# Kernel tuning notes

Hardware: AMD Instinct MI355X
Metric: run time of the kernel (lower is better)

## Reference

```python
import jax, jax.numpy as jnp
import numpy as np

B, S, T1, V = 32, 60, 60, 50000   # batch, post len, response len (decoder runs T1-1 steps), vocab
E, A, H, ATT, DI = 300, 300, 512, 512, 512  # word emb, affect emb, rnn hidden, attention size, decoder input


def setup_inputs() -> dict:
    key = jax.random.key(0)
    ks = jax.random.split(key, 20)
    p = lambda i, shape: jax.random.normal(ks[i], shape, jnp.float32) * 0.02
    z = lambda n: jnp.zeros((n,), jnp.float32)
    return {
        'posts': jax.random.randint(ks[0], (B, S), 0, V),
        'responses': jax.random.randint(ks[1], (B, T1), 0, V),
        'len_posts': jnp.full((B,), S, jnp.int32),
        'emb': p(2, (V, E)), 'affect_emb': p(3, (V, A)),
        'enc_Wi': p(4, (3 * H, E)), 'enc_Wh': p(5, (3 * H, H)), 'enc_bi': z(3 * H), 'enc_bh': z(3 * H),
        'aff_Wi': p(6, (3 * H, A)), 'aff_Wh': p(7, (3 * H, H)), 'aff_bi': z(3 * H), 'aff_bh': z(3 * H),
        'Wp': p(8, (H, 2 * H)), 'bp': z(H),
        'Wl': p(9, (DI, E + H + ATT)), 'bl': z(DI),
        'dec_Wi': p(10, (3 * H, DI)), 'dec_Wh': p(11, (3 * H, H)), 'dec_bi': z(3 * H), 'dec_bh': z(3 * H),
        'Wa': p(12, (H, H)), 'Wc': p(13, (ATT, H)), 'bc': z(ATT),
        'Wv': p(14, (V, H + ATT)), 'bv': z(V),
    }


def _gru_cell(x, h, Wi, Wh, bi, bh):
    gi = x @ Wi.T + bi
    gh = h @ Wh.T + bh
    ir, iz, inn = jnp.split(gi, 3, -1)
    hr, hz, hn = jnp.split(gh, 3, -1)
    r = jax.nn.sigmoid(ir + hr)
    zg = jax.nn.sigmoid(iz + hz)
    n = jnp.tanh(inn + r * hn)
    return (1.0 - zg) * n + zg * h


def _gru_seq(xs, h0, Wi, Wh, bi, bh):
    # xs: [S, B, in] -> (outputs [S,B,H], h_last [B,H])
    def step(h, x):
        h2 = _gru_cell(x, h, Wi, Wh, bi, bh)
        return h2, h2
    hT, ys = jax.lax.scan(step, h0, xs)
    return ys, hT


def reference(posts, responses, len_posts, emb, affect_emb,
              enc_Wi, enc_Wh, enc_bi, enc_bh,
              aff_Wi, aff_Wh, aff_bi, aff_bh,
              Wp, bp, Wl, bl,
              dec_Wi, dec_Wh, dec_bi, dec_bh,
              Wa, Wc, bc, Wv, bv):
    embed_posts = emb[posts]            # [B,S,E]
    affect_posts = affect_emb[posts]    # [B,S,A]
    h0 = jnp.zeros((posts.shape[0], H), embed_posts.dtype)

    _, state_encoder = _gru_seq(embed_posts.transpose(1, 0, 2), h0, enc_Wi, enc_Wh, enc_bi, enc_bh)
    out_affect, state_affect = _gru_seq(affect_posts.transpose(1, 0, 2), h0, aff_Wi, aff_Wh, aff_bi, aff_bh)
    context_affect = out_affect[-1]     # [B,H] (all lengths == S)
    K = out_affect.transpose(1, 0, 2)   # [B,S,H] attention keys/values

    # PrepareState: Linear + tanh on concat of both encoder final states
    state0 = jnp.tanh(jnp.concatenate([state_encoder, state_affect], -1) @ Wp.T + bp)

    dec_in = emb[responses[:, :-1]].transpose(1, 0, 2)  # [T,B,E]
    init_attn = jnp.zeros((posts.shape[0], ATT), embed_posts.dtype)

    def dec_step(carry, x_emb):
        h, attn = carry
        x = jnp.concatenate([x_emb, context_affect, attn], -1) @ Wl.T + bl
        h = _gru_cell(x, h, dec_Wi, dec_Wh, dec_bi, dec_bh)
        scores = jnp.einsum('bd,bsd->bs', h @ Wa, K)        # Luong 'general'
        w = jax.nn.softmax(scores, -1)
        ctx = jnp.einsum('bs,bsd->bd', w, K)
        attn = jnp.tanh(ctx @ Wc.T + bc)
        return (h, attn), (jnp.concatenate([h, attn], -1), w)

    _, (outs, weights) = jax.lax.scan(dec_step, (state0, init_attn), dec_in)
    outs = outs.transpose(1, 0, 2)          # [B,T,H+ATT]
    weights = weights.transpose(1, 0, 2)    # [B,T,S]
    output_vocab = jax.nn.softmax(outs @ Wv.T + bv, -1)  # [B,T,V]
    return output_vocab, weights
```

## Files before the change

### kernel.cpp

```cpp
#include <hip/hip_runtime.h>

typedef unsigned int uint32;
typedef unsigned short u16;
typedef unsigned long long u64;
typedef __attribute__((ext_vector_type(8))) short bf8;
typedef __attribute__((ext_vector_type(4))) float f4;
typedef __attribute__((ext_vector_type(4))) uint32 u32x4;

#define DEV static __device__ __forceinline__

DEV f4 MFMA(bf8 a, bf8 b, f4 c) {
  return __builtin_amdgcn_mfma_f32_16x16x32_bf16(a, b, c, 0, 0, 0);
}
DEV u16 f2bf(float f) {
  uint32 u = __float_as_uint(f);
  return (u16)((u + 0x7FFFu + ((u >> 16) & 1u)) >> 16);
}
DEV float bf2f(u16 h) { return __uint_as_float(((uint32)h) << 16); }
DEV float bfLO(uint32 u) { return __uint_as_float(u << 16); }
DEV float bfHI(uint32 u) { return __uint_as_float(u & 0xFFFF0000u); }
DEV float sigmoid_(float x) { return 1.f / (1.f + __expf(-x)); }
DEV float tanh_(float x) {
  float cx = fminf(fmaxf(x, -15.f), 15.f);
  float e = __expf(2.f * cx);
  return (e - 1.f) / (e + 1.f);
}

DEV u64 ldA64(const void* p) {
  return __hip_atomic_load((u64*)p, __ATOMIC_RELAXED, __HIP_MEMORY_SCOPE_AGENT);
}
DEV void stA64(void* p, u64 v) {
  __hip_atomic_store((u64*)p, v, __ATOMIC_RELAXED, __HIP_MEMORY_SCOPE_AGENT);
}
DEV void stA32(int* p, int v) {
  __hip_atomic_store(p, v, __ATOMIC_RELAXED, __HIP_MEMORY_SCOPE_AGENT);
}
DEV bf8 pk_frag(u64 lo, u64 hi) {
  u32x4 v = {(uint32)lo, (uint32)(lo >> 32), (uint32)hi, (uint32)(hi >> 32)};
  return __builtin_bit_cast(bf8, v);
}

DEV void wait_vm0() { asm volatile("s_waitcnt vmcnt(0)" ::: "memory"); }
DEV void wait_slots(const int* slots, int n, int tgt) {
  const int lane = threadIdx.x & 63;
  for (int i = 0; i < (1 << 20); ++i) {
    int v = 0x7fffffff;
    if (lane < n)
      v = __hip_atomic_load((int*)(slots + lane), __ATOMIC_RELAXED,
                            __HIP_MEMORY_SCOPE_AGENT);
    if (__all(v >= tgt)) return;
    __builtin_amdgcn_s_sleep(1);
  }
}

namespace L {
constexpr size_t o_flags  = 0;
constexpr size_t o_rowsum = 4096;
constexpr size_t o_bcomb  = 11776;
constexpr size_t o_gistat = 17920;
constexpr size_t o_xbuf   = 214528;
constexpr size_t o_henc   = 345600;
constexpr size_t o_haff   = 411136;
constexpr size_t o_cat    = 476672;
constexpr size_t o_Kbuf   = 542208;
constexpr size_t o_KA     = 2508288;
constexpr size_t o_embP   = 4474368;
constexpr size_t o_embA   = 5703168;
constexpr size_t o_embD   = 6931968;
constexpr size_t o_encWi  = 8140288;
constexpr size_t o_affWi  = 9123328;
constexpr size_t o_Whe    = 10106368;
constexpr size_t o_Wha    = 11679232;
constexpr size_t o_decWi  = 13252096;
constexpr size_t o_WlT    = 14824960;
constexpr size_t o_Wa     = 16184832;
constexpr size_t o_Wp     = 16709120;
constexpr size_t o_wq     = 17757696;
constexpr size_t o_Wcomb  = 18281984;
constexpr size_t o_WdE    = 26441216;
constexpr size_t o_WdA    = 27424256;
constexpr size_t o_Wd2    = 28997120;
constexpr size_t o_giE    = 32142848;
constexpr size_t o_giA    = 43939328;
constexpr size_t o_giD    = 55735808;
constexpr size_t o_outsB  = 67335680;
constexpr size_t o_WvB    = 71267840;
constexpr size_t WS_FULL  = 174028288;
constexpr size_t WOFF = 94400000;
}

__global__ __launch_bounds__(256) void kp_gather(
    const int* __restrict__ posts, const int* __restrict__ resp,
    const float* __restrict__ emb, const float* __restrict__ aemb, char* ws)
{
  using namespace L;
  const int gid = blockIdx.x * 256 + threadIdx.x;
  const int r = gid / 320, e = gid - r * 320;
  u16* embP = (u16*)(ws + o_embP);
  u16* embA = (u16*)(ws + o_embA);
  u16* embD = (u16*)(ws + o_embD);
  if (r < 1920) {
    const int b = r & 31, s = r >> 5;
    const int tok = posts[b * 60 + s];
    embP[r * 320 + e] = f2bf(e < 300 ? emb[(size_t)tok * 300 + e] : 0.f);
    embA[r * 320 + e] = f2bf(e < 300 ? aemb[(size_t)tok * 300 + e] : 0.f);
  } else if (r < 3808) {
    const int r2 = r - 1920;
    const int b = r2 & 31, t = r2 >> 5;
    const int tok = resp[b * 60 + t];
    embD[r2 * 320 + e] = f2bf(e < 300 ? emb[(size_t)tok * 300 + e] : 0.f);
  }
}

__global__ __launch_bounds__(256) void kp_wconv(
    const float* __restrict__ encWi, const float* __restrict__ affWi,
    const float* __restrict__ encWh, const float* __restrict__ affWh,
    const float* __restrict__ dWi, const float* __restrict__ Wl,
    const float* __restrict__ Wa, const float* __restrict__ Wp,
    const float* __restrict__ Wc, char* ws)
{
  using namespace L;
  long gid = (long)blockIdx.x * 256 + threadIdx.x;
  if (gid < 983040) {
    const int g = gid >= 491520;
    const long u = gid - (g ? 491520 : 0);
    const int n = (int)(u / 320), e = (int)(u - (long)n * 320);
    const float* src = g ? affWi : encWi;
    u16* dst = (u16*)(ws + (g ? o_affWi : o_encWi));
    dst[u] = f2bf(e < 300 ? src[(size_t)n * 300 + e] : 0.f);
    return;
  }
  gid -= 983040;
  if (gid < 2359296) {
    const int g = (int)(gid / 786432);
    const long u = gid - (long)g * 786432;
    const float* src = g == 0 ? encWh : (g == 1 ? affWh : dWi);
    u16* dst = (u16*)(ws + (g == 0 ? o_Whe : (g == 1 ? o_Wha : o_decWi)));
    dst[u] = f2bf(src[u]);
    return;
  }
  gid -= 2359296;
  if (gid < 679936) {
    const int j = (int)(gid >> 9), k = (int)(gid & 511);
    ((u16*)(ws + o_WlT))[gid] = f2bf(j < 1324 ? Wl[(size_t)k * 1324 + j] : 0.f);
    return;
  }
  gid -= 679936;
  if (gid < 262144) { ((u16*)(ws + o_Wa))[gid] = f2bf(Wa[gid]); return; }
  gid -= 262144;
  if (gid < 524288) { ((u16*)(ws + o_Wp))[gid] = f2bf(Wp[gid]); return; }
  gid -= 524288;
  if (gid < 131072) {
    const int q = (int)(gid & 3), j = (int)((gid >> 2) & 511), g4 = (int)(gid >> 11);
    const int d0 = g4 * 8 + q * 2;
    const uint32 lo = f2bf(Wc[(size_t)j * 512 + d0]);
    const uint32 hi = f2bf(Wc[(size_t)j * 512 + d0 + 1]);
    ((uint32*)(ws + o_wq))[gid] = lo | (hi << 16);
    return;
  }
  gid -= 131072;
  if (gid < 2944) {
    if (gid < 1024) ((uint32*)(ws + o_flags))[gid] = 0;
    else ((uint32*)(ws + o_rowsum))[gid - 1024] = 0;
    return;
  }
  gid -= 2944;
  if (gid < 49152) {
    if (gid < 16384) ((uint32*)(ws + o_outsB + (size_t)1888 * 1024 * 2))[gid] = 0;
    else if (gid < 32768) ((uint32*)(ws + o_henc))[gid - 16384] = 0;
    else ((uint32*)(ws + o_haff))[gid - 32768] = 0;
  }
}

__global__ __launch_bounds__(256) void kp_bcomb(
    const float* __restrict__ dWi, const float* __restrict__ bl,
    const float* __restrict__ dbi, char* ws)
{
  const int i = blockIdx.x * 256 + threadIdx.x;
  if (i >= 1536) return;
  float a = dbi[i];
  for (int k = 0; k < 512; ++k) a += dWi[(size_t)i * 512 + k] * bl[k];
  ((float*)(ws + L::o_bcomb))[i] = a;
}

__global__ __launch_bounds__(256) void kp_wv(const float* __restrict__ Wv, char* ws)
{
  const long gid = (long)blockIdx.x * 256 + threadIdx.x;
  const int r = (int)(gid >> 8), q = (int)(gid & 255);
  u16* WvB = (u16*)(ws + L::o_WvB);
  uint2 o;
  if (r < 50000) {
    const float4 f = *(const float4*)(Wv + (size_t)r * 1024 + q * 4);
    o.x = (uint32)f2bf(f.x) | ((uint32)f2bf(f.y) << 16);
    o.y = (uint32)f2bf(f.z) | ((uint32)f2bf(f.w) << 16);
  } else { o.x = 0u; o.y = 0u; }
  *(uint2*)(WvB + (size_t)r * 1024 + q * 4) = o;
}

__global__ __launch_bounds__(256) void kp_pack2(
    const float* __restrict__ Wcomb, const float* __restrict__ dWh, char* ws)
{
  using namespace L;
  long gid = (long)blockIdx.x * 256 + threadIdx.x;
  if (gid < 491520) {
    const int n = (int)(gid / 320), e = (int)(gid - (long)n * 320);
    ((u16*)(ws + o_WdE))[gid] = f2bf(e < 300 ? Wcomb[(size_t)n * 1328 + e] : 0.f);
    return;
  }
  gid -= 491520;
  if (gid < 786432) {
    const int n = (int)(gid >> 9), k = (int)(gid & 511);
    ((u16*)(ws + o_WdA))[gid] = f2bf(Wcomb[(size_t)n * 1328 + 300 + k]);
    return;
  }
  gid -= 786432;
  if (gid < 1572864) {
    const int n = (int)(gid >> 10), k = (int)(gid & 1023);
    const float v = (k < 512) ? Wcomb[(size_t)n * 1328 + 812 + k]
                              : dWh[(size_t)n * 512 + (k - 512)];
    ((u16*)(ws + o_Wd2))[gid] = f2bf(v);
  }
}

__global__ __launch_bounds__(256) void k_gemm_nt(
    const u16* __restrict__ A, const u16* __restrict__ Bm,
    float* __restrict__ C, const float* __restrict__ bias,
    const int M, const int N, const int Kp)
{
  const int mt = blockIdx.x, cb = blockIdx.y;
  const int w = threadIdx.x >> 6, lane = threadIdx.x & 63;
  const int l15 = lane & 15, lhi = lane >> 4;
  const u16* arow = A + (size_t)(mt * 16 + l15) * Kp + lhi * 8;
  const int c0 = cb * 256 + w * 64;
  f4 acc[4];
#pragma unroll
  for (int nn = 0; nn < 4; ++nn) acc[nn] = (f4){0.f, 0.f, 0.f, 0.f};
  for (int k = 0; k < Kp; k += 32) {
    const bf8 a = *(const bf8*)(arow + k);
#pragma unroll
    for (int nn = 0; nn < 4; ++nn) {
      const int cs = c0 + nn * 16;
      if (cs < N) {
        const bf8 b = *(const bf8*)(Bm + (size_t)(cs + l15) * Kp + k + lhi * 8);
        acc[nn] = MFMA(a, b, acc[nn]);
      }
    }
  }
#pragma unroll
  for (int nn = 0; nn < 4; ++nn) {
    const int cs = c0 + nn * 16;
    if (cs >= N) continue;
    const int c = cs + l15;
    const float bb = bias ? bias[c] : 0.f;
#pragma unroll
    for (int j = 0; j < 4; ++j) {
      const int r = mt * 16 + lhi * 4 + j;
      C[(size_t)r * N + c] = acc[nn][j] + bb;
    }
  }
}

__global__ __launch_bounds__(256, 1) void k_enc(
    char* __restrict__ ws, const float* __restrict__ enc_bh,
    const float* __restrict__ aff_bh)
{
  using namespace L;
  const int tid = threadIdx.x, blk = blockIdx.x;
  const int wave = tid >> 6, lane = tid & 63;
  const int l15 = lane & 15, lhi = lane >> 4;
  const int g = blk >> 5;
  const bool act = wave < 2;
  int* flags = (int*)(ws + o_flags);
  int* slotE = flags + 128 + g * 64;
  const u16* Wh = (const u16*)(ws + (g ? o_Wha : o_Whe));
  const float* gi = (const float*)(ws + (g ? o_giA : o_giE));
  const float* bh = g ? aff_bh : enc_bh;
  u16* hbuf = (u16*)(ws + (g ? o_haff : o_henc));
  u16* cat = (u16*)(ws + o_cat);
  u16* Kb = (u16*)(ws + o_Kbuf);

  const int wid = (blk & 31) * 2 + (wave & 1);
  const int btile = wid >> 5, ctile = wid & 31;
  const int bl = btile * 16 + l15;
  const int c0 = ctile * 16 + lhi * 4;
  const u16* wr0 = Wh + (size_t)(ctile * 16 + l15) * 512 + lhi * 8;
  const u16* wr1 = wr0 + (size_t)512 * 512;
  const u16* wr2 = wr1 + (size_t)512 * 512;
  f4 bhr4 = {0.f, 0.f, 0.f, 0.f}, bhz4 = bhr4, bhn4 = bhr4;
  if (act) {
    bhr4 = *(const f4*)(bh + c0);
    bhz4 = *(const f4*)(bh + 512 + c0);
    bhn4 = *(const f4*)(bh + 1024 + c0);
  }
  for (int s = 0; s < 60; ++s) {
    const u16* hin = hbuf + (s & 1) * (32 * 512);
    u16* hout = hbuf + ((s & 1) ^ 1) * (32 * 512);
    if (act) {
      const u16* brow = hin + bl * 512 + lhi * 8;
      u64 flo[16], fhi[16];
#pragma unroll
      for (int kk = 0; kk < 16; ++kk) {
        flo[kk] = ldA64(brow + kk * 32);
        fhi[kk] = ldA64(brow + kk * 32 + 4);
      }
      const u64 hq = ldA64(hin + bl * 512 + c0);
      f4 ar = {0.f, 0.f, 0.f, 0.f}, az = ar, an = ar;
#pragma unroll
      for (int kk = 0; kk < 16; ++kk) {
        const bf8 hf = pk_frag(flo[kk], fhi[kk]);
        ar = MFMA(*(const bf8*)(wr0 + kk * 32), hf, ar);
        az = MFMA(*(const bf8*)(wr1 + kk * 32), hf, az);
        an = MFMA(*(const bf8*)(wr2 + kk * 32), hf, an);
      }
      const float* gr = gi + (size_t)(s * 32 + bl) * 1536;
      const f4 g0 = *(const f4*)(gr + c0);
      const f4 g1 = *(const f4*)(gr + 512 + c0);
      const f4 g2 = *(const f4*)(gr + 1024 + c0);
      u64 pk = 0;
#pragma unroll
      for (int j = 0; j < 4; ++j) {
        const float r = sigmoid_(g0[j] + ar[j] + bhr4[j]);
        const float z = sigmoid_(g1[j] + az[j] + bhz4[j]);
        const float n = tanh_(g2[j] + r * (an[j] + bhn4[j]));
        const float hold = bf2f((u16)(hq >> (16 * j)));
        pk |= (u64)f2bf((1.f - z) * n + z * hold) << (16 * j);
      }
      stA64(hout + bl * 512 + c0, pk);
      if (g) *(u64*)(Kb + (size_t)(s * 32 + bl) * 512 + c0) = pk;
      if (s == 59) *(u64*)(cat + bl * 1024 + g * 512 + c0) = pk;
    }
    wait_vm0();
    __syncthreads();
    if (tid == 0) stA32(&slotE[blk & 31], s + 1);
    if (wave == 2) wait_slots(slotE, 32, s + 1);
    __syncthreads();
  }
}

__global__ __launch_bounds__(256) void k_mid(char* __restrict__ ws,
                                             const float* __restrict__ bp)
{
  using namespace L;
  const int tid = threadIdx.x, blk = blockIdx.x;
  const int wave = tid >> 6, lane = tid & 63;
  const int l15 = lane & 15, lhi = lane >> 4;
  u16* xb = (u16*)(ws + o_xbuf);
  u16* cat = (u16*)(ws + o_cat);
  u16* Kb = (u16*)(ws + o_Kbuf);

  if (blk < 16) {
    const u16* Wp_ = (const u16*)(ws + o_Wp);
    const int wid = blk * 4 + wave;
    const int btile = wid >> 5, ctile = wid & 31;
    const int bl = btile * 16 + l15;
    const int c0 = ctile * 16 + lhi * 4;
    const u16* arow = Wp_ + (size_t)(ctile * 16 + l15) * 1024 + lhi * 8;
    const u16* brow = cat + bl * 1024 + lhi * 8;
    f4 acc = {0.f, 0.f, 0.f, 0.f};
    for (int k = 0; k < 1024; k += 32)
      acc = MFMA(*(const bf8*)(arow + k), *(const bf8*)(brow + k), acc);
    const f4 bp4 = *(const f4*)(bp + c0);
    u64 pk = 0;
#pragma unroll
    for (int j = 0; j < 4; ++j)
      pk |= (u64)f2bf(tanh_(acc[j] + bp4[j])) << (16 * j);
    *(u64*)(xb + bl * 1024 + 512 + c0) = pk;
    *(u64*)(xb + bl * 1024 + c0) = 0;
  } else if (blk < 32) {
    const u16* WdA = (const u16*)(ws + o_WdA);
    const float* bco = (const float*)(ws + o_bcomb);
    float* gst = (float*)(ws + o_gistat);
    const int wid = (blk - 16) * 4 + wave;
    const int btile = wid >> 5, ctb = wid & 31;
    const int bl = btile * 16 + l15;
    const int c0 = ctb * 16 + lhi * 4;
    const u16* brow = cat + bl * 1024 + 512 + lhi * 8;
    const u16* a0p = WdA + (size_t)(ctb * 16 + l15) * 512 + lhi * 8;
    const u16* a1p = a0p + (size_t)512 * 512;
    const u16* a2p = a1p + (size_t)512 * 512;
    f4 a0 = {0.f, 0.f, 0.f, 0.f}, a1 = a0, a2 = a0;
    for (int k = 0; k < 512; k += 32) {
      const bf8 bfr = *(const bf8*)(brow + k);
      a0 = MFMA(*(const bf8*)(a0p + k), bfr, a0);
      a1 = MFMA(*(const bf8*)(a1p + k), bfr, a1);
      a2 = MFMA(*(const bf8*)(a2p + k), bfr, a2);
    }
    const f4 v0 = *(const f4*)(bco + c0);
    const f4 v1 = *(const f4*)(bco + 512 + c0);
    const f4 v2 = *(const f4*)(bco + 1024 + c0);
    *(f4*)(gst + bl * 1536 + c0) = a0 + v0;
    *(f4*)(gst + bl * 1536 + 512 + c0) = a1 + v1;
    *(f4*)(gst + bl * 1536 + 1024 + c0) = a2 + v2;
  } else {
    const u16* Wa_ = (const u16*)(ws + o_Wa);
    u16* KAp = (u16*)(ws + o_KA);
    const int widK = (blk - 32) * 4 + wave;
    for (int task = widK; task < 3840; task += 192) {
      const int mt = task >> 5, ct = task & 31;
      const int m = mt * 16 + l15;
      const int c0 = ct * 16 + lhi * 4;
      const u16* arow = Wa_ + (size_t)(ct * 16 + l15) * 512 + lhi * 8;
      const u16* brow = Kb + (size_t)m * 512 + lhi * 8;
      f4 acc = {0.f, 0.f, 0.f, 0.f};
      for (int k = 0; k < 512; k += 32)
        acc = MFMA(*(const bf8*)(arow + k), *(const bf8*)(brow + k), acc);
      u64 pk = 0;
#pragma unroll
      for (int j = 0; j < 4; ++j) pk |= (u64)f2bf(acc[j]) << (16 * j);
      *(u64*)(KAp + (size_t)m * 512 + c0) = pk;
    }
  }
}

__global__ __launch_bounds__(256, 1) void k_dec(
    char* __restrict__ ws, float* __restrict__ out,
    const float* __restrict__ dec_bh, const float* __restrict__ bc)
{
  using namespace L;
  const int tid = threadIdx.x, blk = blockIdx.x;
  const int wave = tid >> 6, lane = tid & 63;
  const int l15 = lane & 15, lhi = lane >> 4;
  int* flags = (int*)(ws + o_flags);
  int* slotA = flags;
  int* slotB = flags + 64;

  __shared__ float hsm[512];
  __shared__ float ctxs[512];
  __shared__ float scb[64];
  __shared__ float wsb[64];
  __shared__ u16 attn_sm[256];

  u16* xb = (u16*)(ws + o_xbuf);
  u16* outs = (u16*)(ws + o_outsB);

  if (blk < 32) {
    const bool act = wave < 2;
    const u16* Wd2 = (const u16*)(ws + o_Wd2);
    const float* gst = (const float*)(ws + o_gistat);
    const float* gD = (const float*)(ws + o_giD);
    const int wid = (blk & 31) * 2 + (wave & 1);
    const int btile = wid >> 5, ctile = wid & 31;
    const int bl = btile * 16 + l15;
    const int c0 = ctile * 16 + lhi * 4;
    const u16* wr = Wd2 + (size_t)(ctile * 16 + l15) * 1024 + lhi * 8;
    const u16* wz = wr + (size_t)512 * 1024;
    const u16* wn = wz + (size_t)512 * 1024;
    f4 bhr4 = {0.f, 0.f, 0.f, 0.f}, bhz4 = bhr4, bhn4 = bhr4;
    f4 s0 = bhr4, s1 = bhr4, s2 = bhr4;
    if (act) {
      bhr4 = *(const f4*)(dec_bh + c0);
      bhz4 = *(const f4*)(dec_bh + 512 + c0);
      bhn4 = *(const f4*)(dec_bh + 1024 + c0);
      s0 = *(const f4*)(gst + bl * 1536 + c0);
      s1 = *(const f4*)(gst + bl * 1536 + 512 + c0);
      s2 = *(const f4*)(gst + bl * 1536 + 1024 + c0);
    }
    for (int t = 0; t < 59; ++t) {
      const u16* xin = xb + (t & 1) * (32 * 1024);
      u16* xout = xb + ((t & 1) ^ 1) * (32 * 1024);
      const u16* brow = xin + bl * 1024 + lhi * 8;
      f4 ar = {0.f, 0.f, 0.f, 0.f}, az = ar, anx = ar, anh = ar;
      u64 hq = 0;
      f4 d0 = ar, d1 = ar, d2 = ar;
      if (t) {
        if (wave == 2) wait_slots(slotA, 32, t);
        __syncthreads();
      }
      if (act) {
        u64 flo[16], fhi[16];
#pragma unroll
        for (int kk = 0; kk < 16; ++kk) {
          flo[kk] = ldA64(brow + (16 + kk) * 32);
          fhi[kk] = ldA64(brow + (16 + kk) * 32 + 4);
        }
        hq = ldA64(xin + bl * 1024 + 512 + c0);
        const float* g2p = gD + (size_t)(t * 32 + bl) * 1536;
        d0 = *(const f4*)(g2p + c0);
        d1 = *(const f4*)(g2p + 512 + c0);
        d2 = *(const f4*)(g2p + 1024 + c0);
#pragma unroll
        for (int kk = 0; kk < 16; ++kk) {
          const bf8 xf = pk_frag(flo[kk], fhi[kk]);
          ar = MFMA(*(const bf8*)(wr + (16 + kk) * 32), xf, ar);
          az = MFMA(*(const bf8*)(wz + (16 + kk) * 32), xf, az);
          anh = MFMA(*(const bf8*)(wn + (16 + kk) * 32), xf, anh);
        }
      }
      if (t) {
        if (wave == 2) wait_slots(slotB, 64, t);
        __syncthreads();
      }
      if (act) {
        u64 glo[16], ghi[16];
#pragma unroll
        for (int kk = 0; kk < 16; ++kk) {
          glo[kk] = ldA64(brow + kk * 32);
          ghi[kk] = ldA64(brow + kk * 32 + 4);
        }
#pragma unroll
        for (int kk = 0; kk < 16; ++kk) {
          const bf8 xf = pk_frag(glo[kk], ghi[kk]);
          ar = MFMA(*(const bf8*)(wr + kk * 32), xf, ar);
          az = MFMA(*(const bf8*)(wz + kk * 32), xf, az);
          anx = MFMA(*(const bf8*)(wn + kk * 32), xf, anx);
        }
        u64 pk = 0;
#pragma unroll
        for (int j = 0; j < 4; ++j) {
          const float r = sigmoid_(s0[j] + d0[j] + ar[j] + bhr4[j]);
          const float z = sigmoid_(s1[j] + d1[j] + az[j] + bhz4[j]);
          const float n = tanh_(s2[j] + d2[j] + anx[j] + r * (anh[j] + bhn4[j]));
          const float hold = bf2f((u16)(hq >> (16 * j)));
          pk |= (u64)f2bf((1.f - z) * n + z * hold) << (16 * j);
        }
        stA64(xout + bl * 1024 + 512 + c0, pk);
        *(u64*)(outs + (size_t)(bl * 59 + t) * 1024 + c0) = pk;
      }
      wait_vm0();
      __syncthreads();
      if (tid == 0) stA32(&slotA[blk], t + 1);
    }
  } else {
    const int idx = blk - 32;
    const int b = idx >> 1, half = idx & 1;
    const u16* KAp = (const u16*)(ws + o_KA);
    const u16* Kb = (const u16*)(ws + o_Kbuf);
    const uint4* wq = (const uint4*)(ws + o_wq);
    for (int t = 0; t < 59; ++t) {
      if (wave == 0) wait_slots(slotA, 32, t + 1);
      __syncthreads();
      const u16* xcur = xb + ((t & 1) ^ 1) * (32 * 1024);
      if (tid < 128) {
        const u64 hv = ldA64(xcur + b * 1024 + 512 + tid * 4);
        const uint32 w0 = (uint32)hv, w1 = (uint32)(hv >> 32);
        hsm[tid * 4 + 0] = bfLO(w0);
        hsm[tid * 4 + 1] = bfHI(w0);
        hsm[tid * 4 + 2] = bfLO(w1);
        hsm[tid * 4 + 3] = bfHI(w1);
      }
      __syncthreads();
      if (tid < 240) {
        const int s = tid >> 2, q = tid & 3;
        const u16* kr = KAp + (size_t)(s * 32 + b) * 512 + q * 128;
        const float* hq = &hsm[q * 128];
        float acc0 = 0.f, acc1 = 0.f;
#pragma unroll 4
        for (int i = 0; i < 128; i += 8) {
          const uint2 k4 = *(const uint2*)(kr + i);
          const uint2 k5 = *(const uint2*)(kr + i + 4);
          const float4 h4 = *(const float4*)(hq + i);
          const float4 h5 = *(const float4*)(hq + i + 4);
          acc0 += h4.x * bfLO(k4.x) + h4.y * bfHI(k4.x)
                + h4.z * bfLO(k4.y) + h4.w * bfHI(k4.y);
          acc1 += h5.x * bfLO(k5.x) + h5.y * bfHI(k5.x)
                + h5.z * bfLO(k5.y) + h5.w * bfHI(k5.y);
        }
        float acc = acc0 + acc1;
        acc += __shfl_xor(acc, 1);
        acc += __shfl_xor(acc, 2);
        if ((tid & 3) == 0) scb[s] = acc;
      }
      __syncthreads();
      if (tid < 64) {
        const float v = (tid < 60) ? scb[tid] : -1e30f;
        float m = v;
#pragma unroll
        for (int d = 1; d < 64; d <<= 1) m = fmaxf(m, __shfl_xor(m, d));
        const float e = (tid < 60) ? __expf(v - m) : 0.f;
        float sm = e;
#pragma unroll
        for (int d = 1; d < 64; d <<= 1) sm += __shfl_xor(sm, d);
        const float w = e / sm;
        if (tid < 60) {
          wsb[tid] = w;
          if (half == 0) out[WOFF + (size_t)(b * 59 + t) * 60 + tid] = w;
        }
      }
      __syncthreads();
      {
        float c0a = 0.f, c0b = 0.f, c1a = 0.f, c1b = 0.f;
#pragma unroll 2
        for (int s = 0; s < 60; s += 2) {
          const float w0 = wsb[s], w1 = wsb[s + 1];
          const u16* kr0 = Kb + (size_t)(s * 32 + b) * 512;
          const u16* kr1 = Kb + (size_t)((s + 1) * 32 + b) * 512;
          c0a += w0 * bf2f(kr0[tid]);
          c1a += w0 * bf2f(kr0[tid + 256]);
          c0b += w1 * bf2f(kr1[tid]);
          c1b += w1 * bf2f(kr1[tid + 256]);
        }
        ctxs[tid] = c0a + c0b;
        ctxs[tid + 256] = c1a + c1b;
      }
      __syncthreads();
      const int jj = half * 256 + tid;
      float faa[4] = {0.f, 0.f, 0.f, 0.f};
      float fbb[4] = {0.f, 0.f, 0.f, 0.f};
#pragma unroll 4
      for (int g4 = 0; g4 < 64; ++g4) {
        const uint4 wv4 = wq[g4 * 512 + jj];
        const float4 ca = *(const float4*)&ctxs[g4 * 8];
        const float4 cb2 = *(const float4*)&ctxs[g4 * 8 + 4];
        faa[g4 & 3] += ca.x * bfLO(wv4.x) + ca.y * bfHI(wv4.x)
                     + ca.z * bfLO(wv4.y) + ca.w * bfHI(wv4.y);
        fbb[g4 & 3] += cb2.x * bfLO(wv4.z) + cb2.y * bfHI(wv4.z)
                     + cb2.z * bfLO(wv4.w) + cb2.w * bfHI(wv4.w);
      }
      const float fa = bc[jj] + faa[0] + faa[1] + faa[2] + faa[3]
                     + fbb[0] + fbb[1] + fbb[2] + fbb[3];
      attn_sm[tid] = f2bf(tanh_(fa));
      __syncthreads();
      if (tid < 64) {
        u16* xout = xb + ((t & 1) ^ 1) * (32 * 1024);
        const u64 pk = (u64)attn_sm[tid * 4] | ((u64)attn_sm[tid * 4 + 1] << 16)
                     | ((u64)attn_sm[tid * 4 + 2] << 32) | ((u64)attn_sm[tid * 4 + 3] << 48);
        const int cc = half * 256 + tid * 4;
        stA64(xout + b * 1024 + cc, pk);
        *(u64*)(outs + (size_t)(b * 59 + t) * 1024 + 512 + cc) = pk;
      }
      wait_vm0();
      __syncthreads();
      if (tid == 0) stA32(&slotB[idx], t + 1);
    }
  }
}

__global__ __launch_bounds__(512, 2) void k_vocab2(
    const u16* __restrict__ A, const u16* __restrict__ Bm,
    const float* __restrict__ bvv, float* __restrict__ out,
    float* __restrict__ rowsum)
{
  __shared__ u16 As[2][128][40];
  __shared__ u16 Bs[2][256][40];
  const int tid = threadIdx.x;
  const int bid = blockIdx.x;
  const int xcd = bid & 7, sub = bid >> 3;
  const int wgid = (xcd < 4 ? xcd * 368 : 4 * 368 + (xcd - 4) * 367) + sub;
  const int mtile = wgid % 15, ntile = wgid / 15;
  const int rbase = mtile * 128, cbase = ntile * 256;

  const int wave = tid >> 6, lane = tid & 63;
  const int l15 = lane & 15, lhi = lane >> 4;
  const int m0 = (wave >> 2) * 64, n0 = (wave & 3) * 64;

  const int sar = tid >> 2, sak = (tid & 3) * 8;
  const u16* gA = A + (size_t)(rbase + sar) * 1024 + sak;
  const u16* gB0 = Bm + (size_t)(cbase + sar) * 1024 + sak;
  const u16* gB1 = Bm + (size_t)(cbase + 128 + sar) * 1024 + sak;

  f4 acc[4][4];
#pragma unroll
  for (int mi = 0; mi < 4; ++mi)
#pragma unroll
    for (int ni = 0; ni < 4; ++ni) acc[mi][ni] = (f4){0.f, 0.f, 0.f, 0.f};

  uint4 ra, rb0, rb1;
  ra = *(const uint4*)(gA);
  rb0 = *(const uint4*)(gB0);
  rb1 = *(const uint4*)(gB1);
  *(uint4*)&As[0][sar][sak] = ra;
  *(uint4*)&Bs[0][sar][sak] = rb0;
  *(uint4*)&Bs[0][128 + sar][sak] = rb1;
  __syncthreads();

  int cur = 0;
#pragma unroll 1
  for (int t = 0; t < 32; ++t) {
    if (t < 31) {
      const int k0 = (t + 1) * 32;
      ra = *(const uint4*)(gA + k0);
      rb0 = *(const uint4*)(gB0 + k0);
      rb1 = *(const uint4*)(gB1 + k0);
    }
    bf8 af[4], bfr[4];
#pragma unroll
    for (int mi = 0; mi < 4; ++mi)
      af[mi] = *(const bf8*)&As[cur][m0 + mi * 16 + l15][lhi * 8];
#pragma unroll
    for (int ni = 0; ni < 4; ++ni)
      bfr[ni] = *(const bf8*)&Bs[cur][n0 + ni * 16 + l15][lhi * 8];
#pragma unroll
    for (int mi = 0; mi < 4; ++mi)
#pragma unroll
      for (int ni = 0; ni < 4; ++ni)
        acc[mi][ni] = MFMA(af[mi], bfr[ni], acc[mi][ni]);
    if (t < 31) {
      __syncthreads();
      *(uint4*)&As[cur ^ 1][sar][sak] = ra;
      *(uint4*)&Bs[cur ^ 1][sar][sak] = rb0;
      *(uint4*)&Bs[cur ^ 1][128 + sar][sak] = rb1;
      __syncthreads();
      cur ^= 1;
    }
  }

#pragma unroll
  for (int mi = 0; mi < 4; ++mi) {
    float rs[4] = {0.f, 0.f, 0.f, 0.f};
#pragma unroll
    for (int ni = 0; ni < 4; ++ni) {
      const int c = cbase + n0 + ni * 16 + l15;
      if (c < 50000) {
        const float bb = bvv[c];
#pragma unroll
        for (int j = 0; j < 4; ++j) {
          const int r = rbase + m0 + mi * 16 + lhi * 4 + j;
          if (r < 1888) {
            const float e = __expf(acc[mi][ni][j] + bb);
            out[(size_t)r * 50000 + c] = e;
            rs[j] += e;
          }
        }
      }
    }
#pragma unroll
    for (int j = 0; j < 4; ++j) {
#pragma unroll
      for (int d = 1; d < 16; d <<= 1) rs[j] += __shfl_xor(rs[j], d);
    }
    if (l15 == 0) {
#pragma unroll
      for (int j = 0; j < 4; ++j) {
        const int r = rbase + m0 + mi * 16 + lhi * 4 + j;
        if (r < 1888) atomicAdd(&rowsum[r], rs[j]);
      }
    }
  }
}

__global__ __launch_bounds__(512) void k_vocab0(
    const u16* __restrict__ A, const float* __restrict__ WvF,
    const float* __restrict__ bv, float* __restrict__ out,
    float* __restrict__ rowsum)
{
  const int bid = blockIdx.x;
  const int x = bid & 7, jj = bid >> 3;
  const int mtile = jj % 15, nseq = jj / 15;
  const int ntile = nseq * 8 + x;
  if (ntile >= 196) return;
  const int w = threadIdx.x >> 6, lane = threadIdx.x & 63;
  const int l15 = lane & 15, lhi = lane >> 4;
  const int rbase = mtile * 128 + w * 16;
  const u16* arow = A + (size_t)(rbase + l15) * 1024 + lhi * 8;
  const int cbase = ntile * 256;
  f4 acc[16];
#pragma unroll
  for (int nn = 0; nn < 16; ++nn) acc[nn] = (f4){0.f, 0.f, 0.f, 0.f};
  for (int k = 0; k < 1024; k += 32) {
    const bf8 a = *(const bf8*)(arow + k);
#pragma unroll
    for (int nn = 0; nn < 16; ++nn) {
      const int cs = cbase + nn * 16;
      bf8 bfr = {0, 0, 0, 0, 0, 0, 0, 0};
      if (cs < 50000) {
        const float* p = WvF + (size_t)(cs + l15) * 1024 + k + lhi * 8;
        const float4 f0 = *(const float4*)p;
        const float4 f1 = *(const float4*)(p + 4);
        bfr[0] = (short)(__float_as_uint(f0.x) >> 16);
        bfr[1] = (short)(__float_as_uint(f0.y) >> 16);
        bfr[2] = (short)(__float_as_uint(f0.z) >> 16);
        bfr[3] = (short)(__float_as_uint(f0.w) >> 16);
        bfr[4] = (short)(__float_as_uint(f1.x) >> 16);
        bfr[5] = (short)(__float_as_uint(f1.y) >> 16);
        bfr[6] = (short)(__float_as_uint(f1.z) >> 16);
        bfr[7] = (short)(__float_as_uint(f1.w) >> 16);
      }
      acc[nn] = MFMA(a, bfr, acc[nn]);
    }
  }
  float rsv[4] = {0.f, 0.f, 0.f, 0.f};
#pragma unroll
  for (int nn = 0; nn < 16; ++nn) {
    const int cs = cbase + nn * 16;
    if (cs >= 50000) continue;
    const int c = cs + l15;
    const float bb = bv[c];
#pragma unroll
    for (int j = 0; j < 4; ++j) {
      const int r = rbase + lhi * 4 + j;
      if (r < 1888) {
        const float e = __expf(acc[nn][j] + bb);
        out[(size_t)r * 50000 + c] = e;
        rsv[j] += e;
      }
    }
  }
#pragma unroll
  for (int j = 0; j < 4; ++j) {
#pragma unroll
    for (int d = 1; d < 16; d <<= 1) rsv[j] += __shfl_xor(rsv[j], d);
  }
  if (l15 == 0) {
#pragma unroll
    for (int j = 0; j < 4; ++j) {
      const int r = rbase + lhi * 4 + j;
      if (r < 1888) atomicAdd(&rowsum[r], rsv[j]);
    }
  }
}

__global__ void k_invrow(float* rs)
{
  const int i = blockIdx.x * 256 + threadIdx.x;
  if (i < 1920) {
    const float s = rs[i];
    rs[i] = (s > 0.f) ? 1.f / s : 0.f;
  }
}

__global__ __launch_bounds__(256) void k_scale(float* __restrict__ out,
                                               const float* __restrict__ inv)
{
  const int bid = blockIdx.x;
  const int r = bid / 49, ch = bid - r * 49;
  const int c = ch * 1024 + threadIdx.x * 4;
  if (c < 50000) {
    const float s = inv[r];
    float4* p = (float4*)(out + (size_t)r * 50000 + c);
    float4 v = *p;
    v.x *= s; v.y *= s; v.z *= s; v.w *= s;
    *p = v;
  }
}

extern "C" void kernel_launch(void* const* d_in, const int* in_sizes, int n_in,
                              void* d_out, int out_size, void* d_ws, size_t ws_size,
                              hipStream_t stream) {
  const int* posts = (const int*)d_in[0];
  const int* resp = (const int*)d_in[1];
  const float* emb = (const float*)d_in[3];
  const float* aemb = (const float*)d_in[4];
  const float* encWi = (const float*)d_in[5];
  const float* encWh = (const float*)d_in[6];
  const float* enc_bi = (const float*)d_in[7];
  const float* enc_bh = (const float*)d_in[8];
  const float* affWi = (const float*)d_in[9];
  const float* affWh = (const float*)d_in[10];
  const float* aff_bi = (const float*)d_in[11];
  const float* aff_bh = (const float*)d_in[12];
  const float* Wp = (const float*)d_in[13];
  const float* bp = (const float*)d_in[14];
  const float* Wl = (const float*)d_in[15];
  const float* bl = (const float*)d_in[16];
  const float* dWi = (const float*)d_in[17];
  const float* dWh = (const float*)d_in[18];
  const float* dbi = (const float*)d_in[19];
  const float* dbh = (const float*)d_in[20];
  const float* Wa = (const float*)d_in[21];
  const float* Wc = (const float*)d_in[22];
  const float* bc = (const float*)d_in[23];
  const float* Wv = (const float*)d_in[24];
  const float* bv = (const float*)d_in[25];
  char* ws = (char*)d_ws;
  float* out = (float*)d_out;
  const bool useWvB = ws_size >= L::WS_FULL;

  kp_gather<<<4760, 256, 0, stream>>>(posts, resp, emb, aemb, ws);
  kp_wconv<<<19500, 256, 0, stream>>>(encWi, affWi, encWh, affWh, dWi, Wl, Wa, Wp, Wc, ws);
  kp_bcomb<<<6, 256, 0, stream>>>(dWi, bl, dbi, ws);
  if (useWvB) kp_wv<<<50176, 256, 0, stream>>>(Wv, ws);

  k_gemm_nt<<<dim3(96, 6), 256, 0, stream>>>(
      (const u16*)(ws + L::o_decWi), (const u16*)(ws + L::o_WlT),
      (float*)(ws + L::o_Wcomb), nullptr, 1536, 1328, 512);
  kp_pack2<<<11136, 256, 0, stream>>>((const float*)(ws + L::o_Wcomb), dWh, ws);

  k_gemm_nt<<<dim3(120, 6), 256, 0, stream>>>(
      (const u16*)(ws + L::o_embP), (const u16*)(ws + L::o_encWi),
      (float*)(ws + L::o_giE), enc_bi, 1920, 1536, 320);
  k_gemm_nt<<<dim3(120, 6), 256, 0, stream>>>(
      (const u16*)(ws + L::o_embA), (const u16*)(ws + L::o_affWi),
      (float*)(ws + L::o_giA), aff_bi, 1920, 1536, 320);
  k_gemm_nt<<<dim3(118, 6), 256, 0, stream>>>(
      (const u16*)(ws + L::o_embD), (const u16*)(ws + L::o_WdE),
      (float*)(ws + L::o_giD), nullptr, 1888, 1536, 320);

  k_enc<<<64, 256, 0, stream>>>(ws, enc_bh, aff_bh);
  k_mid<<<80, 256, 0, stream>>>(ws, bp);
  k_dec<<<96, 256, 0, stream>>>(ws, out, dbh, bc);

  if (useWvB)
    k_vocab2<<<2940, 512, 0, stream>>>(
        (const u16*)(ws + L::o_outsB), (const u16*)(ws + L::o_WvB),
        bv, out, (float*)(ws + L::o_rowsum));
  else
    k_vocab0<<<2944, 512, 0, stream>>>(
        (const u16*)(ws + L::o_outsB), Wv, bv, out, (float*)(ws + L::o_rowsum));

  k_invrow<<<8, 256, 0, stream>>>((float*)(ws + L::o_rowsum));
  k_scale<<<92512, 256, 0, stream>>>(out, (const float*)(ws + L::o_rowsum));
}
```

Baseline: 2.574 ms.

## Overlap encoder recurrence with decoder-input GEMM and Wv conversion in one launch

Merges the gather, weight-conversion and bias-combination prep kernels into a single launch. It also batches the two encoder input GEMMs into one z-indexed grid. The encoder recurrence now shares a launch with extra blocks that compute the decoder-input GEMM and the Wv bf16 conversion, so that work fills idle CUs while the 64 recurrent blocks spin on flags. The decoder outputs move to a time-major layout, with the row permutation applied in the vocab epilogue, and the inverse row-sum kernel is folded into the scale kernel. The risk is that co-scheduled blocks compete with the latency-critical recurrent blocks or delay their residency; the spin-wait limit was doubled to allow for this.

Result: no change. 2.570 ms, median of 2 (-0.2%).

```diff
diff --git a/kernel.cpp b/kernel.cpp
--- a/kernel.cpp
+++ b/kernel.cpp
@@ -43,7 +43,7 @@
 DEV void wait_vm0() { asm volatile("s_waitcnt vmcnt(0)" ::: "memory"); }
 DEV void wait_slots(const int* slots, int n, int tgt) {
   const int lane = threadIdx.x & 63;
-  for (int i = 0; i < (1 << 20); ++i) {
+  for (int i = 0; i < (1 << 21); ++i) {
     int v = 0x7fffffff;
     if (lane < n)
       v = __hip_atomic_load((int*)(slots + lane), __ATOMIC_RELAXED,
@@ -89,38 +89,37 @@
 constexpr size_t WOFF = 94400000;
 }
 
-__global__ __launch_bounds__(256) void kp_gather(
+__global__ __launch_bounds__(256) void kp_all(
     const int* __restrict__ posts, const int* __restrict__ resp,
-    const float* __restrict__ emb, const float* __restrict__ aemb, char* ws)
-{
-  using namespace L;
-  const int gid = blockIdx.x * 256 + threadIdx.x;
-  const int r = gid / 320, e = gid - r * 320;
-  u16* embP = (u16*)(ws + o_embP);
-  u16* embA = (u16*)(ws + o_embA);
-  u16* embD = (u16*)(ws + o_embD);
-  if (r < 1920) {
-    const int b = r & 31, s = r >> 5;
-    const int tok = posts[b * 60 + s];
-    embP[r * 320 + e] = f2bf(e < 300 ? emb[(size_t)tok * 300 + e] : 0.f);
-    embA[r * 320 + e] = f2bf(e < 300 ? aemb[(size_t)tok * 300 + e] : 0.f);
-  } else if (r < 3808) {
-    const int r2 = r - 1920;
-    const int b = r2 & 31, t = r2 >> 5;
-    const int tok = resp[b * 60 + t];
-    embD[r2 * 320 + e] = f2bf(e < 300 ? emb[(size_t)tok * 300 + e] : 0.f);
-  }
-}
-
-__global__ __launch_bounds__(256) void kp_wconv(
+    const float* __restrict__ emb, const float* __restrict__ aemb,
     const float* __restrict__ encWi, const float* __restrict__ affWi,
     const float* __restrict__ encWh, const float* __restrict__ affWh,
     const float* __restrict__ dWi, const float* __restrict__ Wl,
     const float* __restrict__ Wa, const float* __restrict__ Wp,
-    const float* __restrict__ Wc, char* ws)
+    const float* __restrict__ Wc, const float* __restrict__ bl,
+    const float* __restrict__ dbi, char* ws)
 {
   using namespace L;
   long gid = (long)blockIdx.x * 256 + threadIdx.x;
+  if (gid < 1218560) {
+    const int r = (int)(gid / 320), e = (int)(gid - (long)r * 320);
+    u16* embP = (u16*)(ws + o_embP);
+    u16* embA = (u16*)(ws + o_embA);
+    u16* embD = (u16*)(ws + o_embD);
+    if (r < 1920) {
+      const int b = r & 31, s = r >> 5;
+      const int tok = posts[b * 60 + s];
+      embP[r * 320 + e] = f2bf(e < 300 ? emb[(size_t)tok * 300 + e] : 0.f);
+      embA[r * 320 + e] = f2bf(e < 300 ? aemb[(size_t)tok * 300 + e] : 0.f);
+    } else if (r < 3808) {
+      const int r2 = r - 1920;
+      const int b = r2 & 31, t = r2 >> 5;
+      const int tok = resp[b * 60 + t];
+      embD[r2 * 320 + e] = f2bf(e < 300 ? emb[(size_t)tok * 300 + e] : 0.f);
+    }
+    return;
+  }
+  gid -= 1218560;
   if (gid < 983040) {
     const int g = gid >= 491520;
     const long u = gid - (g ? 491520 : 0);
@@ -169,32 +168,15 @@
     if (gid < 16384) ((uint32*)(ws + o_outsB + (size_t)1888 * 1024 * 2))[gid] = 0;
     else if (gid < 32768) ((uint32*)(ws + o_henc))[gid - 16384] = 0;
     else ((uint32*)(ws + o_haff))[gid - 32768] = 0;
-  }
-}
-
-__global__ __launch_bounds__(256) void kp_bcomb(
-    const float* __restrict__ dWi, const float* __restrict__ bl,
-    const float* __restrict__ dbi, char* ws)
-{
-  const int i = blockIdx.x * 256 + threadIdx.x;
-  if (i >= 1536) return;
-  float a = dbi[i];
-  for (int k = 0; k < 512; ++k) a += dWi[(size_t)i * 512 + k] * bl[k];
-  ((float*)(ws + L::o_bcomb))[i] = a;
-}
-
-__global__ __launch_bounds__(256) void kp_wv(const float* __restrict__ Wv, char* ws)
-{
-  const long gid = (long)blockIdx.x * 256 + threadIdx.x;
-  const int r = (int)(gid >> 8), q = (int)(gid & 255);
-  u16* WvB = (u16*)(ws + L::o_WvB);
-  uint2 o;
-  if (r < 50000) {
-    const float4 f = *(const float4*)(Wv + (size_t)r * 1024 + q * 4);
-    o.x = (uint32)f2bf(f.x) | ((uint32)f2bf(f.y) << 16);
-    o.y = (uint32)f2bf(f.z) | ((uint32)f2bf(f.w) << 16);
-  } else { o.x = 0u; o.y = 0u; }
-  *(uint2*)(WvB + (size_t)r * 1024 + q * 4) = o;
+    return;
+  }
+  gid -= 49152;
+  if (gid < 1536) {
+    const int i = (int)gid;
+    float a = dbi[i];
+    for (int k = 0; k < 512; ++k) a += dWi[(size_t)i * 512 + k] * bl[k];
+    ((float*)(ws + L::o_bcomb))[i] = a;
+  }
 }
 
 __global__ __launch_bounds__(256) void kp_pack2(
@@ -260,80 +242,159 @@
   }
 }
 
-__global__ __launch_bounds__(256, 1) void k_enc(
+__global__ __launch_bounds__(256) void k_gemm_gi(
+    char* __restrict__ ws, const float* __restrict__ enc_bi,
+    const float* __restrict__ aff_bi)
+{
+  using namespace L;
+  const int z = blockIdx.z;
+  const u16* A = (const u16*)(ws + (z ? o_embA : o_embP));
+  const u16* Bm = (const u16*)(ws + (z ? o_affWi : o_encWi));
+  float* C = (float*)(ws + (z ? o_giA : o_giE));
+  const float* bias = z ? aff_bi : enc_bi;
+  const int Kp = 320, N = 1536;
+  const int mt = blockIdx.x, cb = blockIdx.y;
+  const int w = threadIdx.x >> 6, lane = threadIdx.x & 63;
+  const int l15 = lane & 15, lhi = lane >> 4;
+  const u16* arow = A + (size_t)(mt * 16 + l15) * Kp + lhi * 8;
+  const int c0 = cb * 256 + w * 64;
+  f4 acc[4];
+#pragma unroll
+  for (int nn = 0; nn < 4; ++nn) acc[nn] = (f4){0.f, 0.f, 0.f, 0.f};
+  for (int k = 0; k < Kp; k += 32) {
+    const bf8 a = *(const bf8*)(arow + k);
+#pragma unroll
+    for (int nn = 0; nn < 4; ++nn) {
+      const bf8 b = *(const bf8*)(Bm + (size_t)(c0 + nn * 16 + l15) * Kp + k + lhi * 8);
+      acc[nn] = MFMA(a, b, acc[nn]);
+    }
+  }
+#pragma unroll
+  for (int nn = 0; nn < 4; ++nn) {
+    const int c = c0 + nn * 16 + l15;
+    const float bb = bias[c];
+#pragma unroll
+    for (int j = 0; j < 4; ++j)
+      C[(size_t)(mt * 16 + lhi * 4 + j) * N + c] = acc[nn][j] + bb;
+  }
+}
+
+__global__ __launch_bounds__(256) void k_encplus(
     char* __restrict__ ws, const float* __restrict__ enc_bh,
-    const float* __restrict__ aff_bh)
+    const float* __restrict__ aff_bh, const float* __restrict__ Wv)
 {
   using namespace L;
   const int tid = threadIdx.x, blk = blockIdx.x;
   const int wave = tid >> 6, lane = tid & 63;
   const int l15 = lane & 15, lhi = lane >> 4;
-  const int g = blk >> 5;
-  const bool act = wave < 2;
-  int* flags = (int*)(ws + o_flags);
-  int* slotE = flags + 128 + g * 64;
-  const u16* Wh = (const u16*)(ws + (g ? o_Wha : o_Whe));
-  const float* gi = (const float*)(ws + (g ? o_giA : o_giE));
-  const float* bh = g ? aff_bh : enc_bh;
-  u16* hbuf = (u16*)(ws + (g ? o_haff : o_henc));
-  u16* cat = (u16*)(ws + o_cat);
-  u16* Kb = (u16*)(ws + o_Kbuf);
-
-  const int wid = (blk & 31) * 2 + (wave & 1);
-  const int btile = wid >> 5, ctile = wid & 31;
-  const int bl = btile * 16 + l15;
-  const int c0 = ctile * 16 + lhi * 4;
-  const u16* wr0 = Wh + (size_t)(ctile * 16 + l15) * 512 + lhi * 8;
-  const u16* wr1 = wr0 + (size_t)512 * 512;
-  const u16* wr2 = wr1 + (size_t)512 * 512;
-  f4 bhr4 = {0.f, 0.f, 0.f, 0.f}, bhz4 = bhr4, bhn4 = bhr4;
-  if (act) {
-    bhr4 = *(const f4*)(bh + c0);
-    bhz4 = *(const f4*)(bh + 512 + c0);
-    bhn4 = *(const f4*)(bh + 1024 + c0);
-  }
-  for (int s = 0; s < 60; ++s) {
-    const u16* hin = hbuf + (s & 1) * (32 * 512);
-    u16* hout = hbuf + ((s & 1) ^ 1) * (32 * 512);
+
+  if (blk < 64) {
+    const int g = blk >> 5;
+    const bool act = wave < 2;
+    int* flags = (int*)(ws + o_flags);
+    int* slotE = flags + 128 + g * 64;
+    const u16* Wh = (const u16*)(ws + (g ? o_Wha : o_Whe));
+    const float* gi = (const float*)(ws + (g ? o_giA : o_giE));
+    const float* bh = g ? aff_bh : enc_bh;
+    u16* hbuf = (u16*)(ws + (g ? o_haff : o_henc));
+    u16* cat = (u16*)(ws + o_cat);
+    u16* Kb = (u16*)(ws + o_Kbuf);
+
+    const int wid = (blk & 31) * 2 + (wave & 1);
+    const int btile = wid >> 5, ctile = wid & 31;
+    const int bl = btile * 16 + l15;
+    const int c0 = ctile * 16 + lhi * 4;
+    const u16* wr0 = Wh + (size_t)(ctile * 16 + l15) * 512 + lhi * 8;
+    const u16* wr1 = wr0 + (size_t)512 * 512;
+    const u16* wr2 = wr1 + (size_t)512 * 512;
+    f4 bhr4 = {0.f, 0.f, 0.f, 0.f}, bhz4 = bhr4, bhn4 = bhr4;
     if (act) {
-      const u16* brow = hin + bl * 512 + lhi * 8;
-      u64 flo[16], fhi[16];
-#pragma unroll
-      for (int kk = 0; kk < 16; ++kk) {
-        flo[kk] = ldA64(brow + kk * 32);
-        fhi[kk] = ldA64(brow + kk * 32 + 4);
-      }
-      const u64 hq = ldA64(hin + bl * 512 + c0);
-      f4 ar = {0.f, 0.f, 0.f, 0.f}, az = ar, an = ar;
-#pragma unroll
-      for (int kk = 0; kk < 16; ++kk) {
-        const bf8 hf = pk_frag(flo[kk], fhi[kk]);
-        ar = MFMA(*(const bf8*)(wr0 + kk * 32), hf, ar);
-        az = MFMA(*(const bf8*)(wr1 + kk * 32), hf, az);
-        an = MFMA(*(const bf8*)(wr2 + kk * 32), hf, an);
-      }
-      const float* gr = gi + (size_t)(s * 32 + bl) * 1536;
-      const f4 g0 = *(const f4*)(gr + c0);
-      const f4 g1 = *(const f4*)(gr + 512 + c0);
-      const f4 g2 = *(const f4*)(gr + 1024 + c0);
-      u64 pk = 0;
-#pragma unroll
-      for (int j = 0; j < 4; ++j) {
-        const float r = sigmoid_(g0[j] + ar[j] + bhr4[j]);
-        const float z = sigmoid_(g1[j] + az[j] + bhz4[j]);
-        const float n = tanh_(g2[j] + r * (an[j] + bhn4[j]));
-        const float hold = bf2f((u16)(hq >> (16 * j)));
-        pk |= (u64)f2bf((1.f - z) * n + z * hold) << (16 * j);
-      }
-      stA64(hout + bl * 512 + c0, pk);
-      if (g) *(u64*)(Kb + (size_t)(s * 32 + bl) * 512 + c0) = pk;
-      if (s == 59) *(u64*)(cat + bl * 1024 + g * 512 + c0) = pk;
-    }
-    wait_vm0();
-    __syncthreads();
-    if (tid == 0) stA32(&slotE[blk & 31], s + 1);
-    if (wave == 2) wait_slots(slotE, 32, s + 1);
-    __syncthreads();
+      bhr4 = *(const f4*)(bh + c0);
+      bhz4 = *(const f4*)(bh + 512 + c0);
+      bhn4 = *(const f4*)(bh + 1024 + c0);
+    }
+    for (int s = 0; s < 60; ++s) {
+      const u16* hin = hbuf + (s & 1) * (32 * 512);
+      u16* hout = hbuf + ((s & 1) ^ 1) * (32 * 512);
+      if (act) {
+        const u16* brow = hin + bl * 512 + lhi * 8;
+        u64 flo[16], fhi[16];
+#pragma unroll
+        for (int kk = 0; kk < 16; ++kk) {
+          flo[kk] = ldA64(brow + kk * 32);
+          fhi[kk] = ldA64(brow + kk * 32 + 4);
+        }
+        const u64 hq = ldA64(hin + bl * 512 + c0);
+        f4 ar = {0.f, 0.f, 0.f, 0.f}, az = ar, an = ar;
+#pragma unroll
+        for (int kk = 0; kk < 16; ++kk) {
+          const bf8 hf = pk_frag(flo[kk], fhi[kk]);
+          ar = MFMA(*(const bf8*)(wr0 + kk * 32), hf, ar);
+          az = MFMA(*(const bf8*)(wr1 + kk * 32), hf, az);
+          an = MFMA(*(const bf8*)(wr2 + kk * 32), hf, an);
+        }
+        const float* gr = gi + (size_t)(s * 32 + bl) * 1536;
+        const f4 g0 = *(const f4*)(gr + c0);
+        const f4 g1 = *(const f4*)(gr + 512 + c0);
+        const f4 g2 = *(const f4*)(gr + 1024 + c0);
+        u64 pk = 0;
+#pragma unroll
+        for (int j = 0; j < 4; ++j) {
+          const float r = sigmoid_(g0[j] + ar[j] + bhr4[j]);
+          const float z = sigmoid_(g1[j] + az[j] + bhz4[j]);
+          const float n = tanh_(g2[j] + r * (an[j] + bhn4[j]));
+          const float hold = bf2f((u16)(hq >> (16 * j)));
+          pk |= (u64)f2bf((1.f - z) * n + z * hold) << (16 * j);
+        }
+        stA64(hout + bl * 512 + c0, pk);
+        if (g) *(u64*)(Kb + (size_t)(s * 32 + bl) * 512 + c0) = pk;
+        if (s == 59) *(u64*)(cat + bl * 1024 + g * 512 + c0) = pk;
+      }
+      wait_vm0();
+      __syncthreads();
+      if (tid == 0) stA32(&slotE[blk & 31], s + 1);
+      if (wave == 2) wait_slots(slotE, 32, s + 1);
+      __syncthreads();
+    }
+  } else if (blk < 772) {
+    const int bb = blk - 64;
+    const int mt = bb % 118, cb = bb / 118;
+    const u16* A = (const u16*)(ws + o_embD);
+    const u16* Bm = (const u16*)(ws + o_WdE);
+    float* C = (float*)(ws + o_giD);
+    const int Kp = 320, N = 1536;
+    const int w = wave;
+    const u16* arow = A + (size_t)(mt * 16 + l15) * Kp + lhi * 8;
+    const int c0 = cb * 256 + w * 64;
+    f4 acc[4];
+#pragma unroll
+    for (int nn = 0; nn < 4; ++nn) acc[nn] = (f4){0.f, 0.f, 0.f, 0.f};
+    for (int k = 0; k < Kp; k += 32) {
+      const bf8 a = *(const bf8*)(arow + k);
+#pragma unroll
+      for (int nn = 0; nn < 4; ++nn) {
+        const bf8 b = *(const bf8*)(Bm + (size_t)(c0 + nn * 16 + l15) * Kp + k + lhi * 8);
+        acc[nn] = MFMA(a, b, acc[nn]);
+      }
+    }
+#pragma unroll
+    for (int nn = 0; nn < 4; ++nn) {
+      const int c = c0 + nn * 16 + l15;
+#pragma unroll
+      for (int j = 0; j < 4; ++j)
+        C[(size_t)(mt * 16 + lhi * 4 + j) * N + c] = acc[nn][j];
+    }
+  } else {
+    const long gid = (long)(blk - 772) * 256 + tid;
+    const int r = (int)(gid >> 8), q = (int)(gid & 255);
+    u16* WvB = (u16*)(ws + o_WvB);
+    uint2 o;
+    if (r < 50000) {
+      const float4 f = *(const float4*)(Wv + (size_t)r * 1024 + q * 4);
+      o.x = (uint32)f2bf(f.x) | ((uint32)f2bf(f.y) << 16);
+      o.y = (uint32)f2bf(f.z) | ((uint32)f2bf(f.w) << 16);
+    } else { o.x = 0u; o.y = 0u; }
+    if (r < 50176) *(uint2*)(WvB + (size_t)r * 1024 + q * 4) = o;
   }
 }
 
@@ -514,7 +575,7 @@
           pk |= (u64)f2bf((1.f - z) * n + z * hold) << (16 * j);
         }
         stA64(xout + bl * 1024 + 512 + c0, pk);
-        *(u64*)(outs + (size_t)(bl * 59 + t) * 1024 + c0) = pk;
+        stA64(outs + (size_t)(t * 32 + bl) * 1024 + c0, pk);
       }
       wait_vm0();
       __syncthreads();
@@ -616,7 +677,7 @@
                      | ((u64)attn_sm[tid * 4 + 2] << 32) | ((u64)attn_sm[tid * 4 + 3] << 48);
         const int cc = half * 256 + tid * 4;
         stA64(xout + b * 1024 + cc, pk);
-        *(u64*)(outs + (size_t)(b * 59 + t) * 1024 + 512 + cc) = pk;
+        stA64(outs + (size_t)(t * 32 + b) * 1024 + 512 + cc, pk);
       }
       wait_vm0();
       __syncthreads();
@@ -625,7 +686,7 @@
   }
 }
 
-__global__ __launch_bounds__(512, 2) void k_vocab2(
+__global__ __launch_bounds__(512, 2) void k_vocab2s(
     const u16* __restrict__ A, const u16* __restrict__ Bm,
     const float* __restrict__ bvv, float* __restrict__ out,
     float* __restrict__ rowsum)
@@ -697,6 +758,14 @@
 #pragma unroll
   for (int mi = 0; mi < 4; ++mi) {
     float rs[4] = {0.f, 0.f, 0.f, 0.f};
+    int ro_[4]; bool rv[4];
+#pragma unroll
+    for (int j = 0; j < 4; ++j) {
+      const int r = rbase + m0 + mi * 16 + lhi * 4 + j;
+      const int tt = r >> 5, bb2 = r & 31;
+      rv[j] = tt < 59;
+      ro_[j] = bb2 * 59 + tt;
+    }
 #pragma unroll
     for (int ni = 0; ni < 4; ++ni) {
       const int c = cbase + n0 + ni * 16 + l15;
@@ -704,10 +773,9 @@
         const float bb = bvv[c];
 #pragma unroll
         for (int j = 0; j < 4; ++j) {
-          const int r = rbase + m0 + mi * 16 + lhi * 4 + j;
-          if (r < 1888) {
+          if (rv[j]) {
             const float e = __expf(acc[mi][ni][j] + bb);
-            out[(size_t)r * 50000 + c] = e;
+            out[(size_t)ro_[j] * 50000 + c] = e;
             rs[j] += e;
           }
         }
@@ -720,10 +788,8 @@
     }
     if (l15 == 0) {
 #pragma unroll
-      for (int j = 0; j < 4; ++j) {
-        const int r = rbase + m0 + mi * 16 + lhi * 4 + j;
-        if (r < 1888) atomicAdd(&rowsum[r], rs[j]);
-      }
+      for (int j = 0; j < 4; ++j)
+        if (rv[j]) atomicAdd(&rowsum[ro_[j]], rs[j]);
     }
   }
 }
@@ -768,54 +834,37 @@
       acc[nn] = MFMA(a, bfr, acc[nn]);
     }
   }
-  float rsv[4] = {0.f, 0.f, 0.f, 0.f};
-#pragma unroll
-  for (int nn = 0; nn < 16; ++nn) {
-    const int cs = cbase + nn * 16;
-    if (cs >= 50000) continue;
-    const int c = cs + l15;
-    const float bb = bv[c];
-#pragma unroll
-    for (int j = 0; j < 4; ++j) {
-      const int r = rbase + lhi * 4 + j;
-      if (r < 1888) {
-        const float e = __expf(acc[nn][j] + bb);
-        out[(size_t)r * 50000 + c] = e;
-        rsv[j] += e;
-      }
-    }
-  }
 #pragma unroll
   for (int j = 0; j < 4; ++j) {
-#pragma unroll
-    for (int d = 1; d < 16; d <<= 1) rsv[j] += __shfl_xor(rsv[j], d);
-  }
-  if (l15 == 0) {
-#pragma unroll
-    for (int j = 0; j < 4; ++j) {
-      const int r = rbase + lhi * 4 + j;
-      if (r < 1888) atomicAdd(&rowsum[r], rsv[j]);
-    }
-  }
-}
-
-__global__ void k_invrow(float* rs)
-{
-  const int i = blockIdx.x * 256 + threadIdx.x;
-  if (i < 1920) {
-    const float s = rs[i];
-    rs[i] = (s > 0.f) ? 1.f / s : 0.f;
+    const int r = rbase + lhi * 4 + j;
+    const int tt = r >> 5, bb2 = r & 31;
+    if (tt >= 59) continue;
+    const int ro = bb2 * 59 + tt;
+    float rsv = 0.f;
+#pragma unroll
+    for (int nn = 0; nn < 16; ++nn) {
+      const int cs = cbase + nn * 16;
+      if (cs >= 50000) continue;
+      const int c = cs + l15;
+      const float e = __expf(acc[nn][j] + bv[c]);
+      out[(size_t)ro * 50000 + c] = e;
+      rsv += e;
+    }
+#pragma unroll
+    for (int d = 1; d < 16; d <<= 1) rsv += __shfl_xor(rsv, d);
+    if (l15 == 0) atomicAdd(&rowsum[ro], rsv);
   }
 }
 
 __global__ __launch_bounds__(256) void k_scale(float* __restrict__ out,
-                                               const float* __restrict__ inv)
+                                               const float* __restrict__ rowsum)
 {
   const int bid = blockIdx.x;
   const int r = bid / 49, ch = bid - r * 49;
   const int c = ch * 1024 + threadIdx.x * 4;
   if (c < 50000) {
-    const float s = inv[r];
+    const float sden = rowsum[r];
+    const float s = (sden > 0.f) ? 1.f / sden : 0.f;
     float4* p = (float4*)(out + (size_t)r * 50000 + c);
     float4 v = *p;
     v.x *= s; v.y *= s; v.z *= s; v.w *= s;
@@ -855,38 +904,29 @@
   float* out = (float*)d_out;
   const bool useWvB = ws_size >= L::WS_FULL;
 
-  kp_gather<<<4760, 256, 0, stream>>>(posts, resp, emb, aemb, ws);
-  kp_wconv<<<19500, 256, 0, stream>>>(encWi, affWi, encWh, affWh, dWi, Wl, Wa, Wp, Wc, ws);
-  kp_bcomb<<<6, 256, 0, stream>>>(dWi, bl, dbi, ws);
-  if (useWvB) kp_wv<<<50176, 256, 0, stream>>>(Wv, ws);
+  kp_all<<<24266, 256, 0, stream>>>(posts, resp, emb, aemb, encWi, affWi,
+                                    encWh, affWh, dWi, Wl, Wa, Wp, Wc, bl,
+                                    dbi, ws);
 
   k_gemm_nt<<<dim3(96, 6), 256, 0, stream>>>(
       (const u16*)(ws + L::o_decWi), (const u16*)(ws + L::o_WlT),
       (float*)(ws + L::o_Wcomb), nullptr, 1536, 1328, 512);
   kp_pack2<<<11136, 256, 0, stream>>>((const float*)(ws + L::o_Wcomb), dWh, ws);
 
-  k_gemm_nt<<<dim3(120, 6), 256, 0, stream>>>(
-      (const u16*)(ws + L::o_embP), (const u16*)(ws + L::o_encWi),
-      (float*)(ws + L::o_giE), enc_bi, 1920, 1536, 320);
-  k_gemm_nt<<<dim3(120, 6), 256, 0, stream>>>(
-      (const u16*)(ws + L::o_embA), (const u16*)(ws + L::o_affWi),
-      (float*)(ws + L::o_giA), aff_bi, 1920, 1536, 320);
-  k_gemm_nt<<<dim3(118, 6), 256, 0, stream>>>(
-      (const u16*)(ws + L::o_embD), (const u16*)(ws + L::o_WdE),
-      (float*)(ws + L::o_giD), nullptr, 1888, 1536, 320);
-
-  k_enc<<<64, 256, 0, stream>>>(ws, enc_bh, aff_bh);
+  k_gemm_gi<<<dim3(120, 6, 2), 256, 0, stream>>>(ws, enc_bi, aff_bi);
+
+  k_encplus<<<useWvB ? 50948 : 772, 256, 0, stream>>>(ws, enc_bh, aff_bh, Wv);
   k_mid<<<80, 256, 0, stream>>>(ws, bp);
+
   k_dec<<<96, 256, 0, stream>>>(ws, out, dbh, bc);
 
   if (useWvB)
-    k_vocab2<<<2940, 512, 0, stream>>>(
+    k_vocab2s<<<2940, 512, 0, stream>>>(
         (const u16*)(ws + L::o_outsB), (const u16*)(ws + L::o_WvB),
         bv, out, (float*)(ws + L::o_rowsum));
   else
     k_vocab0<<<2944, 512, 0, stream>>>(
         (const u16*)(ws + L::o_outsB), Wv, bv, out, (float*)(ws + L::o_rowsum));
 
-  k_invrow<<<8, 256, 0, stream>>>((float*)(ws + L::o_rowsum));
   k_scale<<<92512, 256, 0, stream>>>(out, (const float*)(ws + L::o_rowsum));
 }
```
